# Kernel tuning notes

Hardware: AMD Instinct MI355X
Metric: run time of the kernel (lower is better)

The kernel has to match this reference:

```python
import jax, jax.numpy as jnp
import numpy as np

H = 1024
A = H // 2
B = 32
S = 1024
T = 1024


def setup_inputs() -> dict:
    key = jax.random.key(0)
    ks = jax.random.split(key, 16)
    sc = 0.02
    inp = {
        "hidden": jax.random.normal(ks[0], (1, B, H), jnp.float32),
        "encoder_hiddens": jax.random.normal(ks[1], (S, B, H), jnp.float32),
        "h0_s": jax.random.normal(ks[2], (T, B, H), jnp.float32),
        "ax": jax.random.uniform(ks[3], (B, S, 1), jnp.float32),
        # weights: torch Linear(in,out,bias=False) -> W has shape [out,in], y = x @ W.T
        "W1": jax.random.normal(ks[4], (A, H), jnp.float32) * sc,
        "W2": jax.random.normal(ks[5], (A, H), jnp.float32) * sc,
        "W3": jax.random.normal(ks[6], (A, 1), jnp.float32) * sc,
        "W4": jax.random.normal(ks[7], (1, 3 * A), jnp.float32) * sc,
        "W5": jax.random.normal(ks[8], (A, H), jnp.float32) * sc,
        "W6": jax.random.normal(ks[9], (A, H), jnp.float32) * sc,
        "W7": jax.random.normal(ks[10], (A, H), jnp.float32) * sc,
        "W8": jax.random.normal(ks[11], (1, 3 * A), jnp.float32) * sc,
        "W9": jax.random.normal(ks[12], (H, H), jnp.float32) * sc,
        "W10": jax.random.normal(ks[13], (H, H), jnp.float32) * sc,
        "W11": jax.random.normal(ks[14], (1, 2 * H), jnp.float32) * sc,
    }
    return inp


def reference(hidden, encoder_hiddens, h0_s, ax,
              W1, W2, W3, W4, W5, W6, W7, W8, W9, W10, W11):
    h = hidden[0]  # [B,H], hidden.squeeze(0)

    # ---- encoder (x) attention with coverage, vectorized over S ----
    wx = jnp.einsum('sbh,ah->sba', encoder_hiddens, W1)          # [S,B,A]
    wxy = h @ W2.T                                               # [B,A]
    # Linear3 on ax[:, j] ([B,1]): outer product with W3 column
    wxr = ax[:, :, 0][:, :, None] * W3[:, 0][None, None, :]       # [B,S,A]
    wxr = jnp.transpose(wxr, (1, 0, 2))                           # [S,B,A]
    cat_x = jnp.tanh(jnp.concatenate(
        [wx, jnp.broadcast_to(wxy, (S,) + wxy.shape), wxr], axis=-1))  # [S,B,3A]
    exi = jnp.einsum('sbc,oc->bso', cat_x, W4)                    # [B,S,1]
    axi = jax.nn.softmax(exi, axis=1)                             # [B,S,1]
    cxi = jnp.einsum('bs,sbh->bh', axi[:, :, 0], encoder_hiddens)  # [B,H]
    ax_new = ax + axi

    # ---- decoder-history (t) attention, vectorized over T ----
    wt = jnp.einsum('tbh,ah->tba', h0_s, W5)                      # [T,B,A]
    wtx = cxi @ W6.T                                              # [B,A]
    wty = h @ W7.T                                                # [B,A]
    Tn = h0_s.shape[0]
    cat_t = jnp.tanh(jnp.concatenate(
        [wt,
         jnp.broadcast_to(wtx, (Tn,) + wtx.shape),
         jnp.broadcast_to(wty, (Tn,) + wty.shape)], axis=-1))     # [T,B,3A]
    eti = jnp.einsum('tbc,oc->bto', cat_t, W8)                    # [B,T,1]
    ati = jax.nn.softmax(eti, axis=1)
    cti = jnp.einsum('bt,tbh->bh', ati[:, :, 0], h0_s)            # [B,H]

    # ---- gated fusion ----
    gxi = jnp.tanh(cxi @ W9.T)
    gti = jnp.tanh(cti @ W10.T)
    zi = jax.nn.sigmoid(jnp.concatenate([cxi, cti], axis=1) @ W11.T)  # [B,1]
    ci = zi * gxi + (1.0 - zi) * gti                              # [B,H]
    return ci, ax_new
```

## Files before the change

### kernel.cpp

```cpp
#include <hip/hip_runtime.h>
#include <hip/hip_bf16.h>

#define HH 1024
#define AA 512
#define BB 32
#define SS 1024
#define TN 1024
#define M_ENC (SS*BB)
#define M_TOT ((SS+TN)*BB)
#define NCH 8

#define ABUF 8192

typedef __attribute__((ext_vector_type(8))) short short8;
typedef __attribute__((ext_vector_type(4))) float f4;

union bfu { __hip_bfloat16 h; unsigned short u; };
__device__ __forceinline__ unsigned int f2bu(float x) {
  bfu t; t.h = __float2bfloat16(x); return (unsigned int)t.u;
}
__device__ __forceinline__ unsigned short f2b(float x) {
  bfu t; t.h = __float2bfloat16(x); return t.u;
}
__device__ __forceinline__ float tanh_fast(float x) {
  float e = __expf(2.f * x);
  return 1.f - 2.f / (e + 1.f);
}

__global__ void wprep(const float* __restrict__ W, unsigned short* __restrict__ Wc) {
  const int t = blockIdx.x * 256 + threadIdx.x;
  const int lane = t & 63;
  const int rg = (t >> 6) & 31;
  const int kb = t >> 11;
  const int row = rg * 16 + (lane & 15);
  const int k = kb * 32 + ((lane >> 4) << 3);
  const float* src = W + (size_t)row * HH + k;
  f4 v0 = *(const f4*)(src);
  f4 v1 = *(const f4*)(src + 4);
  short8 o;
  o[0] = f2b(v0[0]); o[1] = f2b(v0[1]); o[2] = f2b(v0[2]); o[3] = f2b(v0[3]);
  o[4] = f2b(v1[0]); o[5] = f2b(v1[1]); o[6] = f2b(v1[2]); o[7] = f2b(v1[3]);
  *(short8*)(Wc + (size_t)t * 8) = o;
}

__global__ void poly_prep(const float* __restrict__ W3, const float* __restrict__ W4,
                          float* __restrict__ C) {
  __shared__ float r1[AA], r3[AA], r5[AA];
  const int a = threadIdx.x;
  const float w = W3[a], u = W4[2 * AA + a];
  const float w2 = w * w;
  r1[a] = u * w;
  r3[a] = u * w * w2;
  r5[a] = u * w * w2 * w2;
  __syncthreads();
  for (int off = 256; off > 0; off >>= 1) {
    if (a < off) { r1[a] += r1[a + off]; r3[a] += r3[a + off]; r5[a] += r5[a + off]; }
    __syncthreads();
  }
  if (a == 0) { C[0] = r1[0]; C[1] = -r3[0] / 3.f; C[2] = r5[0] * (2.f / 15.f); }
}

__global__ __launch_bounds__(512, 4)
void e1_gemm(const float* __restrict__ enc, const float* __restrict__ h0,
             const unsigned short* __restrict__ W1c, const unsigned short* __restrict__ W5c,
             const float* __restrict__ W4, const float* __restrict__ W8,
             float* __restrict__ e1s, float* __restrict__ e1t) {
  const int wg   = blockIdx.x;
  const int tid  = threadIdx.x;
  const int lane = tid & 63;
  const int colg = tid >> 6;
  const int l15  = lane & 15;
  const int lg   = lane >> 4;

  const bool is_enc = (wg * 64) < M_ENC;
  const float* __restrict__ Xg = is_enc ? enc : h0;
  const unsigned short* __restrict__ Wc = is_enc ? W1c : W5c;
  const float* __restrict__ Vg = is_enc ? W4 : W8;
  const int row0 = is_enc ? wg * 64 : wg * 64 - M_ENC;

  __shared__ char lds_raw[2 * ABUF];
  float* lred = (float*)lds_raw;

  f4 acc[4][4];
#pragma unroll
  for (int i = 0; i < 4; ++i)
#pragma unroll
    for (int j = 0; j < 4; ++j) acc[i][j] = (f4){0.f, 0.f, 0.f, 0.f};

  const int arow = tid >> 3;
  const int aq   = tid & 7;
  const float* ap = Xg + (size_t)(row0 + arow) * HH + aq * 4;
  const int slotS = (aq >> 1) ^ ((arow >> 1) & 3);
  const int aDst = arow * 64 + slotS * 16 + (aq & 1) * 8;

  const int aRd = l15 * 64 + ((lg ^ ((l15 >> 1) & 3)) << 4);

  const char* bp = (const char*)Wc + colg * 4096 + lane * 16;

  f4 an0, an1;
  short8 bfr[8];

#define ALOAD(k_) do {                                                        \
    an0 = *(const f4*)(ap + (k_) * 64);                                       \
    an1 = *(const f4*)(ap + (k_) * 64 + 32);                                  \
  } while (0)

#define AWR(bo_) do {                                                         \
    uint2 o0_, o1_;                                                           \
    o0_.x = f2bu(an0[0]) | (f2bu(an0[1]) << 16);                              \
    o0_.y = f2bu(an0[2]) | (f2bu(an0[3]) << 16);                              \
    o1_.x = f2bu(an1[0]) | (f2bu(an1[1]) << 16);                              \
    o1_.y = f2bu(an1[2]) | (f2bu(an1[3]) << 16);                              \
    *(uint2*)(lds_raw + (bo_) + aDst) = o0_;                                  \
    *(uint2*)(lds_raw + (bo_) + 4096 + aDst) = o1_;                           \
  } while (0)

#define BLOAD(kb2_) do {                                                      \
    const char* b_ = bp + (size_t)(kb2_) * 65536;                             \
    _Pragma("unroll")                                                         \
    for (int q_ = 0; q_ < 8; ++q_)                                            \
      bfr[q_] = *(const short8*)(b_ + (q_ >> 2) * 32768 + (q_ & 3) * 1024);   \
  } while (0)

#define COMPUTE(bo_) do {                                                     \
    const char* base_ = lds_raw + (bo_);                                      \
    _Pragma("unroll")                                                         \
    for (int ks_ = 0; ks_ < 2; ++ks_) {                                       \
      __builtin_amdgcn_s_setprio(1);                                          \
      _Pragma("unroll")                                                       \
      for (int rt = 0; rt < 4; ++rt) {                                        \
        short8 af_ = *(const short8*)(base_ + ks_ * 4096 + aRd + rt * 1024);  \
        _Pragma("unroll")                                                     \
        for (int cf = 0; cf < 4; ++cf)                                        \
          acc[rt][cf] = __builtin_amdgcn_mfma_f32_16x16x32_bf16(              \
              af_, bfr[ks_ * 4 + cf], acc[rt][cf], 0, 0, 0);                  \
      }                                                                       \
      __builtin_amdgcn_s_setprio(0);                                          \
    }                                                                         \
  } while (0)

#define SYNCA() do {                                                          \
    __builtin_amdgcn_sched_barrier(0);                                        \
    asm volatile("s_waitcnt lgkmcnt(0)" ::: "memory");                        \
    __builtin_amdgcn_s_barrier();                                             \
    __builtin_amdgcn_sched_barrier(0);                                        \
  } while (0)

  ALOAD(0);
  AWR(0);
  ALOAD(1);
  SYNCA();

#pragma unroll 1
  for (int it = 0; it < 7; ++it) {
    AWR(ABUF); ALOAD(2 * it + 2); BLOAD(2 * it); COMPUTE(0); SYNCA();
    AWR(0); ALOAD(2 * it + 3); BLOAD(2 * it + 1); COMPUTE(ABUF); SYNCA();
  }
  AWR(ABUF); BLOAD(14); COMPUTE(0); SYNCA();
  BLOAD(15); COMPUTE(ABUF);
#undef ALOAD
#undef AWR
#undef BLOAD
#undef COMPUTE
#undef SYNCA

  float vvv[4];
#pragma unroll
  for (int cf = 0; cf < 4; ++cf) vvv[cf] = Vg[colg * 64 + cf * 16 + l15];

  __syncthreads();
#pragma unroll
  for (int rt = 0; rt < 4; ++rt) {
    float ps[4] = {0.f, 0.f, 0.f, 0.f};
#pragma unroll
    for (int cf = 0; cf < 4; ++cf) {
      const float w = vvv[cf];
#pragma unroll
      for (int r = 0; r < 4; ++r) ps[r] += w * tanh_fast(acc[rt][cf][r]);
    }
#pragma unroll
    for (int r = 0; r < 4; ++r) {
#pragma unroll
      for (int off = 1; off < 16; off <<= 1) ps[r] += __shfl_xor(ps[r], off);
    }
    if (l15 == 0) {
#pragma unroll
      for (int r = 0; r < 4; ++r)
        lred[colg * 64 + rt * 16 + lg * 4 + r] = ps[r];
    }
  }
  __syncthreads();
  if (tid < 64) {
    float s = 0.f;
#pragma unroll
    for (int c = 0; c < 8; ++c) s += lred[c * 64 + tid];
    const int gr = row0 + tid;
    const int q = gr >> 5;
    const int b = gr & 31;
    if (is_enc) e1s[b * SS + q] = s;
    else        e1t[b * TN + q] = s;
  }
}

__global__ void softmax_bs(const float* __restrict__ e1s, const float* __restrict__ ax,
                           const float* __restrict__ C,
                           float* __restrict__ wout, float* __restrict__ axnew) {
  const int b = blockIdx.x, tid = threadIdx.x;
  const float c0 = C[0], c1 = C[1], c2 = C[2];
  __shared__ float red[256];
  float loc[4], xv[4];
  float m = -1e30f;
#pragma unroll
  for (int i = 0; i < 4; ++i) {
    const int s = i * 256 + tid;
    const float x = ax[b * SS + s];
    const float x2 = x * x;
    xv[i] = x;
    loc[i] = e1s[b * SS + s] + x * (c0 + x2 * (c1 + x2 * c2));
    m = fmaxf(m, loc[i]);
  }
  red[tid] = m; __syncthreads();
  for (int off = 128; off > 0; off >>= 1) {
    if (tid < off) red[tid] = fmaxf(red[tid], red[tid + off]);
    __syncthreads();
  }
  m = red[0]; __syncthreads();
  float sum = 0.f;
#pragma unroll
  for (int i = 0; i < 4; ++i) { loc[i] = __expf(loc[i] - m); sum += loc[i]; }
  red[tid] = sum; __syncthreads();
  for (int off = 128; off > 0; off >>= 1) {
    if (tid < off) red[tid] += red[tid + off];
    __syncthreads();
  }
  const float inv = 1.f / red[0];
#pragma unroll
  for (int i = 0; i < 4; ++i) {
    const int s = i * 256 + tid;
    const float a_ = loc[i] * inv;
    wout[b * SS + s] = a_;
    axnew[b * SS + s] = xv[i] + a_;
  }
}

__global__ void softmax_tb(const float* __restrict__ e1t, float* __restrict__ wout) {
  const int b = blockIdx.x, tid = threadIdx.x;
  __shared__ float red[256];
  float loc[4];
  float m = -1e30f;
#pragma unroll
  for (int i = 0; i < 4; ++i) { loc[i] = e1t[b * TN + i * 256 + tid]; m = fmaxf(m, loc[i]); }
  red[tid] = m; __syncthreads();
  for (int off = 128; off > 0; off >>= 1) {
    if (tid < off) red[tid] = fmaxf(red[tid], red[tid + off]);
    __syncthreads();
  }
  m = red[0]; __syncthreads();
  float sum = 0.f;
#pragma unroll
  for (int i = 0; i < 4; ++i) { loc[i] = __expf(loc[i] - m); sum += loc[i]; }
  red[tid] = sum; __syncthreads();
  for (int off = 128; off > 0; off >>= 1) {
    if (tid < off) red[tid] += red[tid + off];
    __syncthreads();
  }
  const float inv = 1.f / red[0];
#pragma unroll
  for (int i = 0; i < 4; ++i) wout[b * TN + (i * 256 + tid)] = loc[i] * inv;
}

__global__ void wpart(const float* __restrict__ X, const float* __restrict__ w,
                      float* __restrict__ part) {
  const int b = blockIdx.x / NCH, ch = blockIdx.x % NCH;
  const int tid = threadIdx.x;
  __shared__ float ws[SS / NCH];
  if (tid < SS / NCH) ws[tid] = w[b * SS + ch * (SS / NCH) + tid];
  __syncthreads();
  f4 acc = (f4){0.f, 0.f, 0.f, 0.f};
  const float* base = X + ((size_t)(ch * (SS / NCH)) * BB + b) * HH + tid * 4;
#pragma unroll 4
  for (int i = 0; i < SS / NCH; ++i) {
    f4 x = *(const f4*)(base + (size_t)i * BB * HH);
    acc += ws[i] * x;
  }
  *(f4*)&part[((size_t)(b * NCH + ch)) * HH + tid * 4] = acc;
}

__global__ void wreduce(const float* __restrict__ part, float* __restrict__ out) {
  const int idx = blockIdx.x * 256 + threadIdx.x;
  const int b = idx / HH, h = idx % HH;
  float s = 0.f;
#pragma unroll
  for (int ch = 0; ch < NCH; ++ch) s += part[((size_t)(b * NCH + ch)) * HH + h];
  out[idx] = s;
}

__global__ void zi_kernel(const float* __restrict__ cxi, const float* __restrict__ cti,
                          const float* __restrict__ W11, float* __restrict__ zi) {
  const int b = blockIdx.x, tid = threadIdx.x;
  float s = 0.f;
  for (int i = tid; i < HH; i += 256) s += cxi[b * HH + i] * W11[i] + cti[b * HH + i] * W11[HH + i];
  __shared__ float red[4];
  for (int off = 32; off > 0; off >>= 1) s += __shfl_down(s, off);
  if ((tid & 63) == 0) red[tid >> 6] = s;
  __syncthreads();
  if (tid == 0) {
    float t = red[0] + red[1] + red[2] + red[3];
    zi[b] = 1.f / (1.f + __expf(-t));
  }
}

__global__ void ci_kernel(const float* __restrict__ cxi, const float* __restrict__ cti,
                          const float* __restrict__ W9, const float* __restrict__ W10,
                          const float* __restrict__ zi, float* __restrict__ out_ci) {
  const int b = blockIdx.x >> 2, hb = blockIdx.x & 3, tid = threadIdx.x;
  const int h = hb * 256 + tid;
  __shared__ float cx[HH], ct[HH];
  for (int i = tid; i < HH; i += 256) { cx[i] = cxi[b * HH + i]; ct[i] = cti[b * HH + i]; }
  __syncthreads();
  const float* __restrict__ w9r  = W9  + (size_t)h * HH;
  const float* __restrict__ w10r = W10 + (size_t)h * HH;
  float gx = 0.f, gt = 0.f;
  for (int k = 0; k < HH; k += 4) {
    f4 a = *(const f4*)(w9r + k);
    f4 c = *(const f4*)(w10r + k);
    gx += cx[k] * a[0] + cx[k + 1] * a[1] + cx[k + 2] * a[2] + cx[k + 3] * a[3];
    gt += ct[k] * c[0] + ct[k + 1] * c[1] + ct[k + 2] * c[2] + ct[k + 3] * c[3];
  }
  const float z = zi[b];
  out_ci[b * HH + h] = z * tanhf(gx) + (1.f - z) * tanhf(gt);
}

extern "C" void kernel_launch(void* const* d_in, const int* in_sizes, int n_in,
                              void* d_out, int out_size, void* d_ws, size_t ws_size,
                              hipStream_t stream) {
  const float* enc = (const float*)d_in[1];
  const float* h0  = (const float*)d_in[2];
  const float* ax  = (const float*)d_in[3];
  const float* W1  = (const float*)d_in[4];
  const float* W3  = (const float*)d_in[6];
  const float* W4  = (const float*)d_in[7];
  const float* W5  = (const float*)d_in[8];
  const float* W8  = (const float*)d_in[11];
  const float* W9  = (const float*)d_in[12];
  const float* W10 = (const float*)d_in[13];
  const float* W11 = (const float*)d_in[14];
  float* out = (float*)d_out;

  float* w = (float*)d_ws;
  unsigned short* W1c = (unsigned short*)w;
  unsigned short* W5c = (unsigned short*)(w + 262144);
  float* partx = w;
  float* partt = w + 262144;
  float* e1s   = w + 524288;
  float* e1t   = w + 557056;
  float* axi   = w + 589824;
  float* ati   = w + 622592;
  float* cxi   = w + 655360;
  float* cti   = w + 688128;
  float* zi    = w + 720896;
  float* Cpoly = w + 720960;

  wprep<<<256, 256, 0, stream>>>(W1, W1c);
  wprep<<<256, 256, 0, stream>>>(W5, W5c);
  poly_prep<<<1, 512, 0, stream>>>(W3, W4, Cpoly);
  e1_gemm<<<M_TOT / 64, 512, 0, stream>>>(enc, h0, W1c, W5c, W4, W8, e1s, e1t);
  softmax_bs<<<BB, 256, 0, stream>>>(e1s, ax, Cpoly, axi, out + BB * HH);
  softmax_tb<<<BB, 256, 0, stream>>>(e1t, ati);
  wpart<<<BB * NCH, 256, 0, stream>>>(enc, axi, partx);
  wpart<<<BB * NCH, 256, 0, stream>>>(h0, ati, partt);
  wreduce<<<BB * HH / 256, 256, 0, stream>>>(partx, cxi);
  wreduce<<<BB * HH / 256, 256, 0, stream>>>(partt, cti);
  zi_kernel<<<BB, 256, 0, stream>>>(cxi, cti, W11, zi);
  ci_kernel<<<BB * 4, 256, 0, stream>>>(cxi, cti, W9, W10, zi, out);
}
```

Baseline: 219.5 us.

## Switch encoder/history GEMM from 16x16x32 to 32x32x16 bf16 MFMA tiles

```diff
diff --git a/kernel.cpp b/kernel.cpp
--- a/kernel.cpp
+++ b/kernel.cpp
@@ -14,6 +14,7 @@
 
 typedef __attribute__((ext_vector_type(8))) short short8;
 typedef __attribute__((ext_vector_type(4))) float f4;
+typedef __attribute__((ext_vector_type(16))) float f16f;
 
 union bfu { __hip_bfloat16 h; unsigned short u; };
 __device__ __forceinline__ unsigned int f2bu(float x) {
@@ -30,10 +31,10 @@
 __global__ void wprep(const float* __restrict__ W, unsigned short* __restrict__ Wc) {
   const int t = blockIdx.x * 256 + threadIdx.x;
   const int lane = t & 63;
-  const int rg = (t >> 6) & 31;
-  const int kb = t >> 11;
-  const int row = rg * 16 + (lane & 15);
-  const int k = kb * 32 + ((lane >> 4) << 3);
+  const int ct = (t >> 6) & 15;
+  const int kb16 = t >> 10;
+  const int row = ct * 32 + (lane & 31);
+  const int k = kb16 * 16 + ((lane >> 5) << 3);
   const float* src = W + (size_t)row * HH + k;
   f4 v0 = *(const f4*)(src);
   f4 v1 = *(const f4*)(src + 4);
@@ -69,8 +70,8 @@
   const int tid  = threadIdx.x;
   const int lane = tid & 63;
   const int colg = tid >> 6;
-  const int l15  = lane & 15;
-  const int lg   = lane >> 4;
+  const int l31  = lane & 31;
+  const int lhi  = lane >> 5;
 
   const bool is_enc = (wg * 64) < M_ENC;
   const float* __restrict__ Xg = is_enc ? enc : h0;
@@ -81,21 +82,23 @@
   __shared__ char lds_raw[2 * ABUF];
   float* lred = (float*)lds_raw;
 
-  f4 acc[4][4];
-#pragma unroll
-  for (int i = 0; i < 4; ++i)
-#pragma unroll
-    for (int j = 0; j < 4; ++j) acc[i][j] = (f4){0.f, 0.f, 0.f, 0.f};
+  f16f acc[2][2];
+#pragma unroll
+  for (int i = 0; i < 2; ++i)
+#pragma unroll
+    for (int j = 0; j < 2; ++j)
+#pragma unroll
+      for (int g = 0; g < 16; ++g) acc[i][j][g] = 0.f;
 
   const int arow = tid >> 3;
   const int aq   = tid & 7;
   const float* ap = Xg + (size_t)(row0 + arow) * HH + aq * 4;
-  const int slotS = (aq >> 1) ^ ((arow >> 1) & 3);
-  const int aDst = arow * 64 + slotS * 16 + (aq & 1) * 8;
-
-  const int aRd = l15 * 64 + ((lg ^ ((l15 >> 1) & 3)) << 4);
-
-  const char* bp = (const char*)Wc + colg * 4096 + lane * 16;
+  const int aDst = (((aq >> 2) * 2 + (arow >> 5)) * 64 +
+                    (arow & 31) + 32 * ((aq >> 1) & 1)) * 16 + (aq & 1) * 8;
+
+  const int aRd = lane * 16;
+
+  const char* bp = (const char*)Wc + colg * 2048 + lane * 16;
 
   f4 an0, an1;
   short8 bfr[8];
@@ -112,31 +115,31 @@
     o1_.x = f2bu(an1[0]) | (f2bu(an1[1]) << 16);                              \
     o1_.y = f2bu(an1[2]) | (f2bu(an1[3]) << 16);                              \
     *(uint2*)(lds_raw + (bo_) + aDst) = o0_;                                  \
-    *(uint2*)(lds_raw + (bo_) + 4096 + aDst) = o1_;                           \
-  } while (0)
-
-#define BLOAD(kb2_) do {                                                      \
-    const char* b_ = bp + (size_t)(kb2_) * 65536;                             \
+    *(uint2*)(lds_raw + (bo_) + aDst + 4096) = o1_;                           \
+  } while (0)
+
+#define BLOAD(kb_) do {                                                       \
+    const char* b_ = bp + (size_t)(kb_) * 65536;                              \
     _Pragma("unroll")                                                         \
-    for (int q_ = 0; q_ < 8; ++q_)                                            \
-      bfr[q_] = *(const short8*)(b_ + (q_ >> 2) * 32768 + (q_ & 3) * 1024);   \
+    for (int kh_ = 0; kh_ < 4; ++kh_) {                                       \
+      bfr[kh_ * 2]     = *(const short8*)(b_ + kh_ * 16384);                  \
+      bfr[kh_ * 2 + 1] = *(const short8*)(b_ + kh_ * 16384 + 1024);           \
+    }                                                                         \
   } while (0)
 
 #define COMPUTE(bo_) do {                                                     \
     const char* base_ = lds_raw + (bo_);                                      \
+    __builtin_amdgcn_s_setprio(1);                                            \
     _Pragma("unroll")                                                         \
-    for (int ks_ = 0; ks_ < 2; ++ks_) {                                       \
-      __builtin_amdgcn_s_setprio(1);                                          \
-      _Pragma("unroll")                                                       \
-      for (int rt = 0; rt < 4; ++rt) {                                        \
-        short8 af_ = *(const short8*)(base_ + ks_ * 4096 + aRd + rt * 1024);  \
-        _Pragma("unroll")                                                     \
-        for (int cf = 0; cf < 4; ++cf)                                        \
-          acc[rt][cf] = __builtin_amdgcn_mfma_f32_16x16x32_bf16(              \
-              af_, bfr[ks_ * 4 + cf], acc[rt][cf], 0, 0, 0);                  \
-      }                                                                       \
-      __builtin_amdgcn_s_setprio(0);                                          \
+    for (int kh_ = 0; kh_ < 4; ++kh_) {                                       \
+      short8 a0_ = *(const short8*)(base_ + (kh_ * 2) * 1024 + aRd);          \
+      short8 a1_ = *(const short8*)(base_ + (kh_ * 2 + 1) * 1024 + aRd);      \
+      acc[0][0] = __builtin_amdgcn_mfma_f32_32x32x16_bf16(a0_, bfr[kh_ * 2],     acc[0][0], 0, 0, 0); \
+      acc[0][1] = __builtin_amdgcn_mfma_f32_32x32x16_bf16(a0_, bfr[kh_ * 2 + 1], acc[0][1], 0, 0, 0); \
+      acc[1][0] = __builtin_amdgcn_mfma_f32_32x32x16_bf16(a1_, bfr[kh_ * 2],     acc[1][0], 0, 0, 0); \
+      acc[1][1] = __builtin_amdgcn_mfma_f32_32x32x16_bf16(a1_, bfr[kh_ * 2 + 1], acc[1][1], 0, 0, 0); \
     }                                                                         \
+    __builtin_amdgcn_s_setprio(0);                                            \
   } while (0)
 
 #define SYNCA() do {                                                          \
@@ -164,29 +167,25 @@
 #undef COMPUTE
 #undef SYNCA
 
-  float vvv[4];
-#pragma unroll
-  for (int cf = 0; cf < 4; ++cf) vvv[cf] = Vg[colg * 64 + cf * 16 + l15];
-
-  __syncthreads();
-#pragma unroll
-  for (int rt = 0; rt < 4; ++rt) {
-    float ps[4] = {0.f, 0.f, 0.f, 0.f};
-#pragma unroll
-    for (int cf = 0; cf < 4; ++cf) {
-      const float w = vvv[cf];
-#pragma unroll
-      for (int r = 0; r < 4; ++r) ps[r] += w * tanh_fast(acc[rt][cf][r]);
+  const float vv0 = Vg[colg * 64 + l31];
+  const float vv1 = Vg[colg * 64 + 32 + l31];
+
+  __syncthreads();
+#pragma unroll
+  for (int rt = 0; rt < 2; ++rt) {
+    float ps[16];
+#pragma unroll
+    for (int g = 0; g < 16; ++g)
+      ps[g] = vv0 * tanh_fast(acc[rt][0][g]) + vv1 * tanh_fast(acc[rt][1][g]);
+#pragma unroll
+    for (int off = 1; off < 32; off <<= 1) {
+#pragma unroll
+      for (int g = 0; g < 16; ++g) ps[g] += __shfl_xor(ps[g], off);
     }
-#pragma unroll
-    for (int r = 0; r < 4; ++r) {
-#pragma unroll
-      for (int off = 1; off < 16; off <<= 1) ps[r] += __shfl_xor(ps[r], off);
-    }
-    if (l15 == 0) {
-#pragma unroll
-      for (int r = 0; r < 4; ++r)
-        lred[colg * 64 + rt * 16 + lg * 4 + r] = ps[r];
+    if (l31 == 0) {
+#pragma unroll
+      for (int g = 0; g < 16; ++g)
+        lred[colg * 64 + rt * 32 + (g & 3) + 8 * (g >> 2) + 4 * lhi] = ps[g];
     }
   }
   __syncthreads();
```

New measurement: 338.0 us. 54.0% more time.

## Merge paired softmax/weighted-sum/reduce launches, fold gate into ci, stagger GEMM K order

Applied to the files above, without the earlier changes.

```diff
diff --git a/kernel.cpp b/kernel.cpp
--- a/kernel.cpp
+++ b/kernel.cpp
@@ -71,6 +71,7 @@
   const int colg = tid >> 6;
   const int l15  = lane & 15;
   const int lg   = lane >> 4;
+  const int koff = (wg & 1) << 3;
 
   const bool is_enc = (wg * 64) < M_ENC;
   const float* __restrict__ Xg = is_enc ? enc : h0;
@@ -146,18 +147,22 @@
     __builtin_amdgcn_sched_barrier(0);                                        \
   } while (0)
 
-  ALOAD(0);
+  ALOAD(koff);
   AWR(0);
-  ALOAD(1);
+  ALOAD((1 + koff) & 15);
   SYNCA();
 
 #pragma unroll 1
   for (int it = 0; it < 7; ++it) {
-    AWR(ABUF); ALOAD(2 * it + 2); BLOAD(2 * it); COMPUTE(0); SYNCA();
-    AWR(0); ALOAD(2 * it + 3); BLOAD(2 * it + 1); COMPUTE(ABUF); SYNCA();
-  }
-  AWR(ABUF); BLOAD(14); COMPUTE(0); SYNCA();
-  BLOAD(15); COMPUTE(ABUF);
+    const int kc0 = (2 * it + koff) & 15;
+    const int ka2 = (2 * it + 2 + koff) & 15;
+    const int kc1 = (2 * it + 1 + koff) & 15;
+    const int ka3 = (2 * it + 3 + koff) & 15;
+    AWR(ABUF); ALOAD(ka2); BLOAD(kc0); COMPUTE(0); SYNCA();
+    AWR(0); ALOAD(ka3); BLOAD(kc1); COMPUTE(ABUF); SYNCA();
+  }
+  AWR(ABUF); BLOAD((14 + koff) & 15); COMPUTE(0); SYNCA();
+  BLOAD((15 + koff) & 15); COMPUTE(ABUF);
 #undef ALOAD
 #undef AWR
 #undef BLOAD
@@ -202,76 +207,84 @@
   }
 }
 
-__global__ void softmax_bs(const float* __restrict__ e1s, const float* __restrict__ ax,
-                           const float* __restrict__ C,
-                           float* __restrict__ wout, float* __restrict__ axnew) {
-  const int b = blockIdx.x, tid = threadIdx.x;
-  const float c0 = C[0], c1 = C[1], c2 = C[2];
+__global__ void softmax_both(const float* __restrict__ e1s, const float* __restrict__ e1t,
+                             const float* __restrict__ ax, const float* __restrict__ C,
+                             float* __restrict__ axi, float* __restrict__ ati,
+                             float* __restrict__ axnew) {
+  const int tid = threadIdx.x;
   __shared__ float red[256];
-  float loc[4], xv[4];
-  float m = -1e30f;
-#pragma unroll
-  for (int i = 0; i < 4; ++i) {
-    const int s = i * 256 + tid;
-    const float x = ax[b * SS + s];
-    const float x2 = x * x;
-    xv[i] = x;
-    loc[i] = e1s[b * SS + s] + x * (c0 + x2 * (c1 + x2 * c2));
-    m = fmaxf(m, loc[i]);
-  }
-  red[tid] = m; __syncthreads();
-  for (int off = 128; off > 0; off >>= 1) {
-    if (tid < off) red[tid] = fmaxf(red[tid], red[tid + off]);
-    __syncthreads();
-  }
-  m = red[0]; __syncthreads();
-  float sum = 0.f;
-#pragma unroll
-  for (int i = 0; i < 4; ++i) { loc[i] = __expf(loc[i] - m); sum += loc[i]; }
-  red[tid] = sum; __syncthreads();
-  for (int off = 128; off > 0; off >>= 1) {
-    if (tid < off) red[tid] += red[tid + off];
-    __syncthreads();
-  }
-  const float inv = 1.f / red[0];
-#pragma unroll
-  for (int i = 0; i < 4; ++i) {
-    const int s = i * 256 + tid;
-    const float a_ = loc[i] * inv;
-    wout[b * SS + s] = a_;
-    axnew[b * SS + s] = xv[i] + a_;
-  }
-}
-
-__global__ void softmax_tb(const float* __restrict__ e1t, float* __restrict__ wout) {
-  const int b = blockIdx.x, tid = threadIdx.x;
-  __shared__ float red[256];
-  float loc[4];
-  float m = -1e30f;
-#pragma unroll
-  for (int i = 0; i < 4; ++i) { loc[i] = e1t[b * TN + i * 256 + tid]; m = fmaxf(m, loc[i]); }
-  red[tid] = m; __syncthreads();
-  for (int off = 128; off > 0; off >>= 1) {
-    if (tid < off) red[tid] = fmaxf(red[tid], red[tid + off]);
-    __syncthreads();
-  }
-  m = red[0]; __syncthreads();
-  float sum = 0.f;
-#pragma unroll
-  for (int i = 0; i < 4; ++i) { loc[i] = __expf(loc[i] - m); sum += loc[i]; }
-  red[tid] = sum; __syncthreads();
-  for (int off = 128; off > 0; off >>= 1) {
-    if (tid < off) red[tid] += red[tid + off];
-    __syncthreads();
-  }
-  const float inv = 1.f / red[0];
-#pragma unroll
-  for (int i = 0; i < 4; ++i) wout[b * TN + (i * 256 + tid)] = loc[i] * inv;
-}
-
-__global__ void wpart(const float* __restrict__ X, const float* __restrict__ w,
-                      float* __restrict__ part) {
-  const int b = blockIdx.x / NCH, ch = blockIdx.x % NCH;
+  if (blockIdx.x < BB) {
+    const int b = blockIdx.x;
+    const float c0 = C[0], c1 = C[1], c2 = C[2];
+    float loc[4], xv[4];
+    float m = -1e30f;
+#pragma unroll
+    for (int i = 0; i < 4; ++i) {
+      const int s = i * 256 + tid;
+      const float x = ax[b * SS + s];
+      const float x2 = x * x;
+      xv[i] = x;
+      loc[i] = e1s[b * SS + s] + x * (c0 + x2 * (c1 + x2 * c2));
+      m = fmaxf(m, loc[i]);
+    }
+    red[tid] = m; __syncthreads();
+    for (int off = 128; off > 0; off >>= 1) {
+      if (tid < off) red[tid] = fmaxf(red[tid], red[tid + off]);
+      __syncthreads();
+    }
+    m = red[0]; __syncthreads();
+    float sum = 0.f;
+#pragma unroll
+    for (int i = 0; i < 4; ++i) { loc[i] = __expf(loc[i] - m); sum += loc[i]; }
+    red[tid] = sum; __syncthreads();
+    for (int off = 128; off > 0; off >>= 1) {
+      if (tid < off) red[tid] += red[tid + off];
+      __syncthreads();
+    }
+    const float inv = 1.f / red[0];
+#pragma unroll
+    for (int i = 0; i < 4; ++i) {
+      const int s = i * 256 + tid;
+      const float a_ = loc[i] * inv;
+      axi[b * SS + s] = a_;
+      axnew[b * SS + s] = xv[i] + a_;
+    }
+  } else {
+    const int b = blockIdx.x - BB;
+    float loc[4];
+    float m = -1e30f;
+#pragma unroll
+    for (int i = 0; i < 4; ++i) { loc[i] = e1t[b * TN + i * 256 + tid]; m = fmaxf(m, loc[i]); }
+    red[tid] = m; __syncthreads();
+    for (int off = 128; off > 0; off >>= 1) {
+      if (tid < off) red[tid] = fmaxf(red[tid], red[tid + off]);
+      __syncthreads();
+    }
+    m = red[0]; __syncthreads();
+    float sum = 0.f;
+#pragma unroll
+    for (int i = 0; i < 4; ++i) { loc[i] = __expf(loc[i] - m); sum += loc[i]; }
+    red[tid] = sum; __syncthreads();
+    for (int off = 128; off > 0; off >>= 1) {
+      if (tid < off) red[tid] += red[tid + off];
+      __syncthreads();
+    }
+    const float inv = 1.f / red[0];
+#pragma unroll
+    for (int i = 0; i < 4; ++i) ati[b * TN + (i * 256 + tid)] = loc[i] * inv;
+  }
+}
+
+__global__ void wpart2(const float* __restrict__ enc, const float* __restrict__ h0,
+                       const float* __restrict__ axi, const float* __restrict__ ati,
+                       float* __restrict__ partx, float* __restrict__ partt) {
+  const int gb = blockIdx.x;
+  const bool isx = gb < BB * NCH;
+  const float* __restrict__ X = isx ? enc : h0;
+  const float* __restrict__ w = isx ? axi : ati;
+  float* __restrict__ part = isx ? partx : partt;
+  const int idx = isx ? gb : gb - BB * NCH;
+  const int b = idx / NCH, ch = idx % NCH;
   const int tid = threadIdx.x;
   __shared__ float ws[SS / NCH];
   if (tid < SS / NCH) ws[tid] = w[b * SS + ch * (SS / NCH) + tid];
@@ -286,38 +299,37 @@
   *(f4*)&part[((size_t)(b * NCH + ch)) * HH + tid * 4] = acc;
 }
 
-__global__ void wreduce(const float* __restrict__ part, float* __restrict__ out) {
+__global__ void wreduce2(const float* __restrict__ partx, const float* __restrict__ partt,
+                         float* __restrict__ cxi, float* __restrict__ cti) {
   const int idx = blockIdx.x * 256 + threadIdx.x;
-  const int b = idx / HH, h = idx % HH;
+  const bool isx = idx < BB * HH;
+  const float* __restrict__ part = isx ? partx : partt;
+  float* __restrict__ outp = isx ? cxi : cti;
+  const int j = isx ? idx : idx - BB * HH;
+  const int b = j / HH, h = j % HH;
   float s = 0.f;
 #pragma unroll
   for (int ch = 0; ch < NCH; ++ch) s += part[((size_t)(b * NCH + ch)) * HH + h];
-  out[idx] = s;
-}
-
-__global__ void zi_kernel(const float* __restrict__ cxi, const float* __restrict__ cti,
-                          const float* __restrict__ W11, float* __restrict__ zi) {
-  const int b = blockIdx.x, tid = threadIdx.x;
-  float s = 0.f;
-  for (int i = tid; i < HH; i += 256) s += cxi[b * HH + i] * W11[i] + cti[b * HH + i] * W11[HH + i];
-  __shared__ float red[4];
-  for (int off = 32; off > 0; off >>= 1) s += __shfl_down(s, off);
-  if ((tid & 63) == 0) red[tid >> 6] = s;
-  __syncthreads();
-  if (tid == 0) {
-    float t = red[0] + red[1] + red[2] + red[3];
-    zi[b] = 1.f / (1.f + __expf(-t));
-  }
+  outp[j] = s;
 }
 
 __global__ void ci_kernel(const float* __restrict__ cxi, const float* __restrict__ cti,
                           const float* __restrict__ W9, const float* __restrict__ W10,
-                          const float* __restrict__ zi, float* __restrict__ out_ci) {
+                          const float* __restrict__ W11, float* __restrict__ out_ci) {
   const int b = blockIdx.x >> 2, hb = blockIdx.x & 3, tid = threadIdx.x;
   const int h = hb * 256 + tid;
   __shared__ float cx[HH], ct[HH];
+  __shared__ float zred[4];
   for (int i = tid; i < HH; i += 256) { cx[i] = cxi[b * HH + i]; ct[i] = cti[b * HH + i]; }
   __syncthreads();
+  float zs = 0.f;
+  for (int i = tid; i < HH; i += 256) zs += cx[i] * W11[i] + ct[i] * W11[HH + i];
+  for (int off = 32; off > 0; off >>= 1) zs += __shfl_down(zs, off);
+  if ((tid & 63) == 0) zred[tid >> 6] = zs;
+  __syncthreads();
+  const float zt = zred[0] + zred[1] + zred[2] + zred[3];
+  const float z = 1.f / (1.f + __expf(-zt));
+
   const float* __restrict__ w9r  = W9  + (size_t)h * HH;
   const float* __restrict__ w10r = W10 + (size_t)h * HH;
   float gx = 0.f, gt = 0.f;
@@ -327,7 +339,6 @@
     gx += cx[k] * a[0] + cx[k + 1] * a[1] + cx[k + 2] * a[2] + cx[k + 3] * a[3];
     gt += ct[k] * c[0] + ct[k + 1] * c[1] + ct[k + 2] * c[2] + ct[k + 3] * c[3];
   }
-  const float z = zi[b];
   out_ci[b * HH + h] = z * tanhf(gx) + (1.f - z) * tanhf(gt);
 }
 
@@ -358,19 +369,14 @@
   float* ati   = w + 622592;
   float* cxi   = w + 655360;
   float* cti   = w + 688128;
-  float* zi    = w + 720896;
-  float* Cpoly = w + 720960;
+  float* Cpoly = w + 720896;
 
   wprep<<<256, 256, 0, stream>>>(W1, W1c);
   wprep<<<256, 256, 0, stream>>>(W5, W5c);
   poly_prep<<<1, 512, 0, stream>>>(W3, W4, Cpoly);
   e1_gemm<<<M_TOT / 64, 512, 0, stream>>>(enc, h0, W1c, W5c, W4, W8, e1s, e1t);
-  softmax_bs<<<BB, 256, 0, stream>>>(e1s, ax, Cpoly, axi, out + BB * HH);
-  softmax_tb<<<BB, 256, 0, stream>>>(e1t, ati);
-  wpart<<<BB * NCH, 256, 0, stream>>>(enc, axi, partx);
-  wpart<<<BB * NCH, 256, 0, stream>>>(h0, ati, partt);
-  wreduce<<<BB * HH / 256, 256, 0, stream>>>(partx, cxi);
-  wreduce<<<BB * HH / 256, 256, 0, stream>>>(partt, cti);
-  zi_kernel<<<BB, 256, 0, stream>>>(cxi, cti, W11, zi);
-  ci_kernel<<<BB * 4, 256, 0, stream>>>(cxi, cti, W9, W10, zi, out);
-}
+  softmax_both<<<2 * BB, 256, 0, stream>>>(e1s, e1t, ax, Cpoly, axi, ati, out + BB * HH);
+  wpart2<<<2 * BB * NCH, 256, 0, stream>>>(enc, h0, axi, ati, partx, partt);
+  wreduce2<<<2 * BB * HH / 256, 256, 0, stream>>>(partx, partt, cxi, cti);
+  ci_kernel<<<BB * 4, 256, 0, stream>>>(cxi, cti, W9, W10, W11, out);
+}
```

Result: no change. 215.7 us (-1.7%).
